# Optimization experiments

Measured on AMD Instinct MI355X. Metric: run time of the kernel, lower is better.

Reference implementation:

```python
import jax, jax.numpy as jnp
import numpy as np

# Module config (init_kwargs): nodes = (64, 64)
NX, NY_NODES = 64, 64


def setup_inputs() -> dict:
    key = jax.random.key(0)
    data = jax.random.normal(key, (4, 3, 1024, 1024), dtype=jnp.float32)
    return {"data": data}


def reference(data):
    B, C, H, W = data.shape
    scale = W // NX                    # = 16
    ny = H // scale                    # grid rows (= 64 here)
    nx = NX
    N = nx * ny                        # num_nodes = 4096
    p = scale - 1                      # original slices x1:x2 with x2=x1+scale-1 -> (scale-1) pixels

    # [B, C, ny, p, nx, p] top-left (scale-1)x(scale-1) sub-patch of each grid cell
    patches = data.reshape(B, C, ny, scale, nx, scale)[:, :, :, :p, :, :p]

    # L1 affinity between vertically / horizontally adjacent patches
    dv = jnp.abs(patches[:, :, 1:] - patches[:, :, :-1]).sum(axis=(1, 3, 5))          # [B, ny-1, nx]
    dh = jnp.abs(patches[:, :, :, :, 1:] - patches[:, :, :, :, :-1]).sum(axis=(1, 3, 5))  # [B, ny, nx-1]

    node = jnp.arange(ny)[:, None] * nx + jnp.arange(nx)[None, :]  # node_id = x + y*nx

    A = jnp.zeros((B, N, N), dtype=data.dtype)
    # vertical edges: self<->up/down
    lo_v = node[1:, :].ravel()   # lower cell of each vertical pair
    hi_v = node[:-1, :].ravel()  # upper cell
    dv_f = dv.reshape(B, -1)
    A = A.at[:, lo_v, hi_v].set(dv_f)   # self -> up
    A = A.at[:, hi_v, lo_v].set(dv_f)   # self -> down
    # horizontal edges: self<->left/right
    le_h = node[:, :-1].ravel()
    ri_h = node[:, 1:].ravel()
    dh_f = dh.reshape(B, -1)
    A = A.at[:, le_h, ri_h].set(dh_f)   # self -> right
    A = A.at[:, ri_h, le_h].set(dh_f)   # self -> left

    return A, data
```

## Files before the change

### kernel.cpp

```cpp
#include <hip/hip_runtime.h>

#define BB 4
#define CC 3
#define HH 1024
#define WW 1024
#define NXG 64
#define SCALE 16
#define PP 15
#define NNODE 4096

typedef float floatx4 __attribute__((ext_vector_type(4)));

static const long long A_ELEMS    = (long long)BB * NNODE * NNODE;
static const long long DATA_ELEMS = (long long)BB * CC * HH * WW;

#define COPY_BLOCKS 512
#define ROW_BLOCKS  (BB * NNODE)

__global__ __launch_bounds__(256) void fused_band_fill(const float* __restrict__ data,
                                                       float* __restrict__ out) {
    if (blockIdx.x < COPY_BLOCKS) {
        long long i = (long long)blockIdx.x * 256 + threadIdx.x;
        const long long stride = (long long)COPY_BLOCKS * 256;
        const floatx4* __restrict__ src = (const floatx4*)data;
        floatx4* dst = (floatx4*)(out + A_ELEMS);
        const long long nvec = DATA_ELEMS / 4;
        for (; i < nvec; i += stride) dst[i] = src[i];
        return;
    }

    const int rb = blockIdx.x - COPY_BLOCKS;
    const int b  = rb >> 12;
    const int n  = rb & (NNODE - 1);
    const int y  = n >> 6;
    const int x  = n & 63;

    const int w    = threadIdx.x >> 6;
    const int lane = threadIdx.x & 63;
    const int r    = lane >> 2;
    const int q    = lane & 3;

    bool valid; int gy, gx; long long delta;
    switch (w) {
        case 0:  valid = (y > 0);  gy = y - 1; gx = x;     delta = (long long)SCALE * WW; break;
        case 1:  valid = (y < 63); gy = y;     gx = x;     delta = (long long)SCALE * WW; break;
        case 2:  valid = (x > 0);  gy = y;     gx = x - 1; delta = SCALE;                 break;
        default: valid = (x < 63); gy = y;     gx = x;     delta = SCALE;                 break;
    }

    float s = 0.f;
    if (valid && r < PP) {
        const float* p0 = data + (((long long)(b * CC)) * HH + (long long)(gy * SCALE + r)) * WW
                               + gx * SCALE + q * 4;
        #pragma unroll
        for (int c = 0; c < CC; ++c) {
            const float* p = p0 + (long long)c * HH * WW;
            const floatx4 a  = *(const floatx4*)p;
            const floatx4 nb = *(const floatx4*)(p + delta);
            float d = fabsf(nb.x - a.x) + fabsf(nb.y - a.y) + fabsf(nb.z - a.z);
            if (q != 3) d += fabsf(nb.w - a.w);
            s += d;
        }
    }
    #pragma unroll
    for (int off = 32; off; off >>= 1) s += __shfl_down(s, off, 64);

    __shared__ float ev[4];
    if (lane == 0) ev[w] = s;
    __syncthreads();

    const float v_up = ev[0], v_dn = ev[1], v_lf = ev[2], v_rt = ev[3];
    const int c_up = (y > 0)  ? n - NXG : -1;
    const int c_dn = (y < 63) ? n + NXG : -1;
    const int c_lf = (x > 0)  ? n - 1   : -1;
    const int c_rt = (x < 63) ? n + 1   : -1;

    float* rowp = out + ((long long)b * NNODE + n) * NNODE;
    #pragma unroll
    for (int k = 0; k < 4; ++k) {
        const int cb = (int)(threadIdx.x + k * 256) << 2;
        const int c0 = cb, c1 = cb + 1, c2 = cb + 2, c3 = cb + 3;
        floatx4 v;
        v.x = (c0 == c_up) ? v_up : (c0 == c_dn) ? v_dn : (c0 == c_lf) ? v_lf : (c0 == c_rt) ? v_rt : 0.f;
        v.y = (c1 == c_up) ? v_up : (c1 == c_dn) ? v_dn : (c1 == c_lf) ? v_lf : (c1 == c_rt) ? v_rt : 0.f;
        v.z = (c2 == c_up) ? v_up : (c2 == c_dn) ? v_dn : (c2 == c_lf) ? v_lf : (c2 == c_rt) ? v_rt : 0.f;
        v.w = (c3 == c_up) ? v_up : (c3 == c_dn) ? v_dn : (c3 == c_lf) ? v_lf : (c3 == c_rt) ? v_rt : 0.f;
        *(floatx4*)(rowp + cb) = v;
    }
}

extern "C" void kernel_launch(void* const* d_in, const int* in_sizes, int n_in,
                              void* d_out, int out_size, void* d_ws, size_t ws_size,
                              hipStream_t stream) {
    const float* data = (const float*)d_in[0];
    float* out = (float*)d_out;
    fused_band_fill<<<COPY_BLOCKS + ROW_BLOCKS, 256, 0, stream>>>(data, out);
}
```

Before: 348.6 us.

## Split edge-affinity computation from dense band fill into separate kernels

A new first kernel computes each vertical and horizontal edge L1 sum exactly once and stores it in a per-node workspace of four floats. A second grid-stride kernel then streams the dense adjacency matrix, reading those four values per row, alongside the existing data copy. This removes the duplicated edge computation and keeps the patch loads and block-wide sync out of the bandwidth-bound write loop. In exchange it adds a second launch and a workspace round trip. The old fused kernel stays as a fallback when the workspace is too small.

After: 364.6 us. +4.6%, slower.

```diff
diff --git a/kernel.cpp b/kernel.cpp
--- a/kernel.cpp
+++ b/kernel.cpp
@@ -14,9 +14,106 @@
 static const long long A_ELEMS    = (long long)BB * NNODE * NNODE;
 static const long long DATA_ELEMS = (long long)BB * CC * HH * WW;
 
+#define NV_PER_B 4032
+#define NH_PER_B 4032
+#define NV_TOT   16128
+#define NE_TOT   32256
+#define EDGE_BLOCKS 8064
+
+#define A_BLOCKS   4096
 #define COPY_BLOCKS 512
-#define ROW_BLOCKS  (BB * NNODE)
+#define NQ 16777216
 
+#define EV_FLOATS (BB * NNODE * 4)
+#define EV_BYTES  (EV_FLOATS * sizeof(float))
+
+__global__ __launch_bounds__(256) void edge_compute(const float* __restrict__ data,
+                                                    float* __restrict__ EV) {
+    const int wave = blockIdx.x * 4 + (threadIdx.x >> 6);
+    const int lane = threadIdx.x & 63;
+    const int r = lane >> 2;
+    const int q = lane & 3;
+
+    int b, y, x, slot_a, slot_b;
+    long long delta;
+    if (wave < NV_TOT) {
+        const int e = wave;
+        b = e / NV_PER_B; const int rem = e - b * NV_PER_B;
+        y = rem >> 6; x = rem & 63;
+        delta = (long long)SCALE * WW;
+        const int n_up = y * NXG + x;
+        const int n_dn = n_up + NXG;
+        slot_a = (b * NNODE + n_up) * 4 + 1;
+        slot_b = (b * NNODE + n_dn) * 4 + 0;
+    } else {
+        const int e = wave - NV_TOT;
+        b = e / NH_PER_B; const int rem = e - b * NH_PER_B;
+        y = rem / 63; x = rem - y * 63;
+        delta = SCALE;
+        const int n_le = y * NXG + x;
+        const int n_ri = n_le + 1;
+        slot_a = (b * NNODE + n_le) * 4 + 3;
+        slot_b = (b * NNODE + n_ri) * 4 + 2;
+    }
+
+    float s = 0.f;
+    if (r < PP) {
+        const float* p0 = data + (((long long)(b * CC)) * HH + (long long)y * SCALE + r) * WW
+                               + x * SCALE + q * 4;
+        #pragma unroll
+        for (int c = 0; c < CC; ++c) {
+            const float* p = p0 + (long long)c * HH * WW;
+            const floatx4 a  = *(const floatx4*)p;
+            const floatx4 nb = *(const floatx4*)(p + delta);
+            float d = fabsf(nb.x - a.x) + fabsf(nb.y - a.y) + fabsf(nb.z - a.z);
+            if (q != 3) d += fabsf(nb.w - a.w);
+            s += d;
+        }
+    }
+    #pragma unroll
+    for (int off = 32; off; off >>= 1) s += __shfl_down(s, off, 64);
+
+    if (lane == 0) {
+        EV[slot_a] = s;
+        EV[slot_b] = s;
+    }
+}
+
+__global__ __launch_bounds__(256) void band_stream(const float* __restrict__ data,
+                                                   const float* __restrict__ EV,
+                                                   float* __restrict__ out) {
+    if (blockIdx.x >= A_BLOCKS) {
+        long long i = (long long)(blockIdx.x - A_BLOCKS) * 256 + threadIdx.x;
+        const long long stride = (long long)COPY_BLOCKS * 256;
+        const floatx4* __restrict__ src = (const floatx4*)data;
+        floatx4* dst = (floatx4*)(out + A_ELEMS);
+        const long long nvec = DATA_ELEMS / 4;
+        for (; i < nvec; i += stride) dst[i] = src[i];
+        return;
+    }
+
+    for (int i = blockIdx.x * 256 + threadIdx.x; i < NQ; i += A_BLOCKS * 256) {
+        const int ng = i >> 10;
+        const int t  = i & 1023;
+        const floatx4 ev = *(const floatx4*)(EV + ((long long)ng << 2));
+        const int n = ng & (NNODE - 1);
+        const int y = n >> 6, x = n & 63;
+        const int c_up = (y > 0)  ? n - NXG : -1;
+        const int c_dn = (y < 63) ? n + NXG : -1;
+        const int c_lf = (x > 0)  ? n - 1   : -1;
+        const int c_rt = (x < 63) ? n + 1   : -1;
+        const int cb = t << 2;
+        const int c0 = cb, c1 = cb + 1, c2 = cb + 2, c3 = cb + 3;
+        floatx4 v;
+        v.x = (c0 == c_up) ? ev.x : (c0 == c_dn) ? ev.y : (c0 == c_lf) ? ev.z : (c0 == c_rt) ? ev.w : 0.f;
+        v.y = (c1 == c_up) ? ev.x : (c1 == c_dn) ? ev.y : (c1 == c_lf) ? ev.z : (c1 == c_rt) ? ev.w : 0.f;
+        v.z = (c2 == c_up) ? ev.x : (c2 == c_dn) ? ev.y : (c2 == c_lf) ? ev.z : (c2 == c_rt) ? ev.w : 0.f;
+        v.w = (c3 == c_up) ? ev.x : (c3 == c_dn) ? ev.y : (c3 == c_lf) ? ev.z : (c3 == c_rt) ? ev.w : 0.f;
+        *(floatx4*)(out + ((long long)i << 2)) = v;
+    }
+}
+
+#define ROW_BLOCKS (BB * NNODE)
 __global__ __launch_bounds__(256) void fused_band_fill(const float* __restrict__ data,
                                                        float* __restrict__ out) {
     if (blockIdx.x < COPY_BLOCKS) {
@@ -28,18 +125,15 @@
         for (; i < nvec; i += stride) dst[i] = src[i];
         return;
     }
-
     const int rb = blockIdx.x - COPY_BLOCKS;
     const int b  = rb >> 12;
     const int n  = rb & (NNODE - 1);
     const int y  = n >> 6;
     const int x  = n & 63;
-
     const int w    = threadIdx.x >> 6;
     const int lane = threadIdx.x & 63;
     const int r    = lane >> 2;
     const int q    = lane & 3;
-
     bool valid; int gy, gx; long long delta;
     switch (w) {
         case 0:  valid = (y > 0);  gy = y - 1; gx = x;     delta = (long long)SCALE * WW; break;
@@ -47,7 +141,6 @@
         case 2:  valid = (x > 0);  gy = y;     gx = x - 1; delta = SCALE;                 break;
         default: valid = (x < 63); gy = y;     gx = x;     delta = SCALE;                 break;
     }
-
     float s = 0.f;
     if (valid && r < PP) {
         const float* p0 = data + (((long long)(b * CC)) * HH + (long long)(gy * SCALE + r)) * WW
@@ -64,17 +157,14 @@
     }
     #pragma unroll
     for (int off = 32; off; off >>= 1) s += __shfl_down(s, off, 64);
-
-    __shared__ float ev[4];
-    if (lane == 0) ev[w] = s;
+    __shared__ float evs[4];
+    if (lane == 0) evs[w] = s;
     __syncthreads();
-
-    const float v_up = ev[0], v_dn = ev[1], v_lf = ev[2], v_rt = ev[3];
+    const float v_up = evs[0], v_dn = evs[1], v_lf = evs[2], v_rt = evs[3];
     const int c_up = (y > 0)  ? n - NXG : -1;
     const int c_dn = (y < 63) ? n + NXG : -1;
     const int c_lf = (x > 0)  ? n - 1   : -1;
     const int c_rt = (x < 63) ? n + 1   : -1;
-
     float* rowp = out + ((long long)b * NNODE + n) * NNODE;
     #pragma unroll
     for (int k = 0; k < 4; ++k) {
@@ -94,5 +184,11 @@
                               hipStream_t stream) {
     const float* data = (const float*)d_in[0];
     float* out = (float*)d_out;
-    fused_band_fill<<<COPY_BLOCKS + ROW_BLOCKS, 256, 0, stream>>>(data, out);
+    if (ws_size >= (size_t)EV_BYTES && d_ws != nullptr) {
+        float* EV = (float*)d_ws;
+        edge_compute<<<EDGE_BLOCKS, 256, 0, stream>>>(data, EV);
+        band_stream<<<A_BLOCKS + COPY_BLOCKS, 256, 0, stream>>>(data, EV, out);
+    } else {
+        fused_band_fill<<<COPY_BLOCKS + ROW_BLOCKS, 256, 0, stream>>>(data, out);
+    }
 }
```
